# Kernel tuning notes

Hardware: AMD Instinct MI355X
Metric: run time of the kernel (lower is better)

## Reference

```python
import jax, jax.numpy as jnp
import numpy as np

N_NODES = 50000
NEG_SLOPE_ATT = 0.2   # PyG GATConv default LeakyReLU slope for attention logits
NEG_SLOPE_ACT = 0.01  # nn.LeakyReLU default between layers


def _add_self_loops(src, dst, n):
    loop = jnp.arange(n, dtype=src.dtype)
    return jnp.concatenate([src, loop]), jnp.concatenate([dst, loop])


def gat_conv(x, W, a_src, a_dst, b, src, dst, n):
    # x: [N, Cin], W: [Cin, Cout], a_src/a_dst: [Cout], b: [Cout]
    h = x @ W                                   # [N, Cout]
    alpha_src = h @ a_src                       # [N]
    alpha_dst = h @ a_dst                       # [N]
    e = jax.nn.leaky_relu(alpha_src[src] + alpha_dst[dst], NEG_SLOPE_ATT)  # [E]
    # segment softmax over incoming edges of each dst node
    m = jax.ops.segment_max(e, dst, num_segments=n)      # [N]
    ex = jnp.exp(e - m[dst])                              # [E]
    s = jax.ops.segment_sum(ex, dst, num_segments=n)      # [N] (>0: self-loops)
    alpha = ex / s[dst]                                   # [E]
    out = jax.ops.segment_sum(h[src] * alpha[:, None], dst, num_segments=n)
    return out + b


def setup_inputs() -> dict:
    key = jax.random.key(0)
    ks = jax.random.split(key, 20)
    n, e = N_NODES, 800000
    cin, h1, h2, cout = 64, 128, 64, 32
    d = {
        "x": jax.random.normal(ks[0], (n, cin), jnp.float32),
        "edge_index": jax.random.randint(ks[1], (2, e), 0, n, jnp.int64),
    }
    dims = [(cin, h1), (h1, h2), (h2, h1), (h1, cout)]
    for i, (ci, co) in enumerate(dims, 1):
        g = 1.0 / np.sqrt(ci)
        d[f"W{i}"] = jax.random.normal(ks[2 + 4 * i], (ci, co), jnp.float32) * g
        d[f"a{i}s"] = jax.random.normal(ks[3 + 4 * i], (co,), jnp.float32) * 0.1
        d[f"a{i}d"] = jax.random.normal(ks[4 + 4 * i], (co,), jnp.float32) * 0.1
        d[f"b{i}"] = jnp.zeros((co,), jnp.float32)
    return d


def reference(x, edge_index, W1, a1s, a1d, b1, W2, a2s, a2d, b2,
              W3, a3s, a3d, b3, W4, a4s, a4d, b4):
    n = x.shape[0]
    src, dst = _add_self_loops(edge_index[0], edge_index[1], n)
    act = lambda t: jax.nn.leaky_relu(t, NEG_SLOPE_ACT)
    h = act(gat_conv(x, W1, a1s, a1d, b1, src, dst, n))
    # dropout is identity at inference
    h = act(gat_conv(h, W2, a2s, a2d, b2, src, dst, n))
    h = act(gat_conv(h, W3, a3s, a3d, b3, src, dst, n))
    return gat_conv(h, W4, a4s, a4d, b4, src, dst, n)
```

## Files before the change

### kernel.cpp

```cpp
#include <hip/hip_runtime.h>
#include <hip/hip_fp16.h>

#define NEG_ATT 0.2f

typedef int v4i __attribute__((ext_vector_type(4)));


__global__ __launch_bounds__(256) void setup_k(int* cnt, int N, int NB,
                                               const float* __restrict__ W1, const float* __restrict__ a1s,
                                               const float* __restrict__ a1d, const float* __restrict__ W3,
                                               const float* __restrict__ a3s, const float* __restrict__ a3d,
                                               float* __restrict__ wa ) {
    int b = blockIdx.x;
    if (b < NB) {
        int i = b * 256 + threadIdx.x;
        if (i < N) cnt[i] = 0;
    } else {
        int t = threadIdx.x;
        int ci = t & 63;
        int which = t >> 6;
        const float* W = (which < 2) ? W1 : W3;
        const float* a = (which == 0) ? a1s : (which == 1) ? a1d : (which == 2) ? a3s : a3d;
        float s = 0.f;
        for (int co = 0; co < 128; ++co) s += W[ci * 128 + co] * a[co];
        wa[t] = s;
    }
}


__global__ __launch_bounds__(256) void scatter_gemv_k(const int* __restrict__ src, const int* __restrict__ dst,
                                                      int* cnt, int* __restrict__ col,
                                                      int E, int SB,
                                                      const float* __restrict__ X,
                                                      const float* __restrict__ was, const float* __restrict__ wad,
                                                      float* __restrict__ as_, float* __restrict__ ad_,
                                                      __half* __restrict__ x16, int N) {
    if (blockIdx.x < SB) {
        int i4 = blockIdx.x * 256 + threadIdx.x;
        int E4 = E >> 2;
        if (i4 < E4) {
            v4i d4 = *(const v4i*)&dst[i4 * 4];
            v4i s4 = *(const v4i*)&src[i4 * 4];
            #pragma unroll
            for (int u = 0; u < 4; ++u) {
                int slot = atomicAdd(&cnt[d4[u]], 1);
                col[(d4[u] << 6) + slot] = s4[u];
            }
        }
        if (blockIdx.x == 0 && threadIdx.x < (E & 3)) {
            int i = (E & ~3) + threadIdx.x;
            int dd = dst[i];
            int slot = atomicAdd(&cnt[dd], 1);
            col[(dd << 6) + slot] = src[i];
        }
    } else {
        int wid  = ((blockIdx.x - SB) * 256 + threadIdx.x) >> 6;
        int lane = threadIdx.x & 63;
        if (wid >= N) return;
        float xv = X[(size_t)wid * 64 + lane];
        x16[(size_t)wid * 64 + lane] = __float2half(xv);
        float s1 = xv * was[lane];
        float s2 = xv * wad[lane];
        #pragma unroll
        for (int off = 32; off; off >>= 1) {
            s1 += __shfl_xor(s1, off);
            s2 += __shfl_xor(s2, off);
        }
        if (lane == 0) { as_[wid] = s1; ad_[wid] = s2; }
    }
}


__global__ __launch_bounds__(256) void gemm_wide_k(const __half* __restrict__ X16, const float* __restrict__ W,
                                                   const float* __restrict__ bias, __half* __restrict__ H16, int N) {
    __shared__ float Xs[128][68];
    __shared__ float Ws[64][128];
    int tid  = threadIdx.x;
    int row0 = blockIdx.x * 128;

    for (int i = tid; i < 2048; i += 256)
        *(float4*)&((float*)Ws)[i * 4] = *(const float4*)&W[i * 4];
    for (int i = tid; i < 2048; i += 256) {
        int r = i >> 4, k4 = i & 15;
        int gr = row0 + r;
        float4 v = {0.f, 0.f, 0.f, 0.f};
        if (gr < N) {
            uint2 pk = *(const uint2*)&X16[(size_t)gr * 64 + k4 * 4];
            float2 f0 = __half22float2(*(__half2*)&pk.x);
            float2 f1 = __half22float2(*(__half2*)&pk.y);
            v = make_float4(f0.x, f0.y, f1.x, f1.y);
        }
        *(float4*)&Xs[r][k4 * 4] = v;
    }
    __syncthreads();

    int ct = tid & 15;
    int rt = tid >> 4;
    float acc[8][8] = {};
    for (int k = 0; k < 64; k += 4) {
        float4 w0a = *(float4*)&Ws[k][ct * 8],     w0b = *(float4*)&Ws[k][ct * 8 + 4];
        float4 w1a = *(float4*)&Ws[k + 1][ct * 8], w1b = *(float4*)&Ws[k + 1][ct * 8 + 4];
        float4 w2a = *(float4*)&Ws[k + 2][ct * 8], w2b = *(float4*)&Ws[k + 2][ct * 8 + 4];
        float4 w3a = *(float4*)&Ws[k + 3][ct * 8], w3b = *(float4*)&Ws[k + 3][ct * 8 + 4];
        #pragma unroll
        for (int i = 0; i < 8; ++i) {
            float4 xv = *(float4*)&Xs[rt + 16 * i][k];
            acc[i][0] += xv.x * w0a.x + xv.y * w1a.x + xv.z * w2a.x + xv.w * w3a.x;
            acc[i][1] += xv.x * w0a.y + xv.y * w1a.y + xv.z * w2a.y + xv.w * w3a.y;
            acc[i][2] += xv.x * w0a.z + xv.y * w1a.z + xv.z * w2a.z + xv.w * w3a.z;
            acc[i][3] += xv.x * w0a.w + xv.y * w1a.w + xv.z * w2a.w + xv.w * w3a.w;
            acc[i][4] += xv.x * w0b.x + xv.y * w1b.x + xv.z * w2b.x + xv.w * w3b.x;
            acc[i][5] += xv.x * w0b.y + xv.y * w1b.y + xv.z * w2b.y + xv.w * w3b.y;
            acc[i][6] += xv.x * w0b.z + xv.y * w1b.z + xv.z * w2b.z + xv.w * w3b.z;
            acc[i][7] += xv.x * w0b.w + xv.y * w1b.w + xv.z * w2b.w + xv.w * w3b.w;
        }
    }

    float bv[8];
    #pragma unroll
    for (int j = 0; j < 8; ++j) bv[j] = bias[ct * 8 + j];

    #pragma unroll
    for (int i = 0; i < 8; ++i) {
        int gr = row0 + rt + 16 * i;
        if (gr < N) {
            float o[8];
            #pragma unroll
            for (int j = 0; j < 8; ++j) {
                float v = acc[i][j] + bv[j];
                o[j] = v > 0.f ? v : 0.01f * v;
            }
            __half2 h0 = __floats2half2_rn(o[0], o[1]);
            __half2 h1 = __floats2half2_rn(o[2], o[3]);
            __half2 h2 = __floats2half2_rn(o[4], o[5]);
            __half2 h3 = __floats2half2_rn(o[6], o[7]);
            uint4 pk = { *(unsigned*)&h0, *(unsigned*)&h1, *(unsigned*)&h2, *(unsigned*)&h3 };
            *(uint4*)&H16[(size_t)gr * 128 + ct * 8] = pk;
        }
    }
}


template <int CIN, int COUT>
__global__ __launch_bounds__(256) void gemm_k(const __half* __restrict__ X16, const float* __restrict__ W,
                                              const float* __restrict__ a_s, const float* __restrict__ a_d,
                                              __half* __restrict__ Hh, float* __restrict__ as_,
                                              float* __restrict__ ad_, int N) {
    constexpr int RB  = (CIN == 128 && COUT == 64) ? 32 : 64;
    constexpr int NCT = COUT / 4;
    constexpr int NRT = 256 / NCT;
    constexpr int RT  = RB / NRT;
    constexpr int XP  = CIN + 4;
    __shared__ float Xs[RB][XP];
    __shared__ float Ws[CIN][COUT];
    int tid  = threadIdx.x;
    int row0 = blockIdx.x * RB;

    for (int i = tid; i < CIN * COUT / 4; i += 256)
        *(float4*)&((float*)Ws)[i * 4] = *(const float4*)&W[i * 4];
    for (int i = tid; i < RB * CIN / 4; i += 256) {
        int r = i / (CIN / 4), k4 = i % (CIN / 4);
        int gr = row0 + r;
        float4 v = {0.f, 0.f, 0.f, 0.f};
        if (gr < N) {
            uint2 pk = *(const uint2*)&X16[(size_t)gr * CIN + k4 * 4];
            float2 f0 = __half22float2(*(__half2*)&pk.x);
            float2 f1 = __half22float2(*(__half2*)&pk.y);
            v = make_float4(f0.x, f0.y, f1.x, f1.y);
        }
        *(float4*)&Xs[r][k4 * 4] = v;
    }
    __syncthreads();

    int ct = tid % NCT;
    int rt = tid / NCT;
    float acc[RT][4] = {};
    for (int k = 0; k < CIN; k += 4) {
        float4 w0 = *(float4*)&Ws[k][ct * 4];
        float4 w1 = *(float4*)&Ws[k + 1][ct * 4];
        float4 w2 = *(float4*)&Ws[k + 2][ct * 4];
        float4 w3 = *(float4*)&Ws[k + 3][ct * 4];
        #pragma unroll
        for (int i = 0; i < RT; ++i) {
            float4 xv = *(float4*)&Xs[rt + i * NRT][k];
            acc[i][0] += xv.x * w0.x + xv.y * w1.x + xv.z * w2.x + xv.w * w3.x;
            acc[i][1] += xv.x * w0.y + xv.y * w1.y + xv.z * w2.y + xv.w * w3.y;
            acc[i][2] += xv.x * w0.z + xv.y * w1.z + xv.z * w2.z + xv.w * w3.z;
            acc[i][3] += xv.x * w0.w + xv.y * w1.w + xv.z * w2.w + xv.w * w3.w;
        }
    }

    float asv[4], adv[4];
    #pragma unroll
    for (int j = 0; j < 4; ++j) { asv[j] = a_s[ct * 4 + j]; adv[j] = a_d[ct * 4 + j]; }

    #pragma unroll
    for (int i = 0; i < RT; ++i) {
        int gr = row0 + rt + i * NRT;
        float s1 = acc[i][0] * asv[0] + acc[i][1] * asv[1] + acc[i][2] * asv[2] + acc[i][3] * asv[3];
        float s2 = acc[i][0] * adv[0] + acc[i][1] * adv[1] + acc[i][2] * adv[2] + acc[i][3] * adv[3];
        #pragma unroll
        for (int off = 1; off < NCT; off <<= 1) {
            s1 += __shfl_xor(s1, off);
            s2 += __shfl_xor(s2, off);
        }
        if (gr < N) {
            __half2 p0 = __floats2half2_rn(acc[i][0], acc[i][1]);
            __half2 p1 = __floats2half2_rn(acc[i][2], acc[i][3]);
            uint2 pk = { *(unsigned*)&p0, *(unsigned*)&p1 };
            *(uint2*)&Hh[(size_t)gr * COUT + ct * 4] = pk;
            if (ct == 0) { as_[gr] = s1; ad_[gr] = s2; }
        }
    }
}


template <int C, int MODE>
__global__ __launch_bounds__(256) void agg_k(const __half* __restrict__ Hg, const float* __restrict__ as_,
                                             const float* __restrict__ ad_, const int* __restrict__ deg,
                                             const int* __restrict__ col, const float* __restrict__ bias,
                                             const float* __restrict__ was, const float* __restrict__ wad,
                                             float* __restrict__ outf, __half* __restrict__ outh,
                                             float* __restrict__ oas, float* __restrict__ oad, int N) {
    __shared__ int2 sw[4][64];
    int wid  = (blockIdx.x * 256 + threadIdx.x) >> 6;
    int lane = threadIdx.x & 63;
    int wvi  = threadIdx.x >> 6;
    if (wid >= N) return;
    float adi = ad_[wid];
    int dg = deg[wid];
    float a0 = 0.f, a1 = 0.f, b0 = 0.f, b1 = 0.f;
    const int sub  = lane >> 5, c32 = lane & 31;
    const int quad = lane >> 4, c16 = lane & 15;

    int s_l = 0; float w_l = 0.f;
    if (lane < dg) {
        s_l = col[(wid << 6) + lane];
        float e = as_[s_l] + adi;
        e = e > 0.f ? e : NEG_ATT * e;
        w_l = __expf(e);
    }
    sw[wvi][lane] = make_int2(s_l, __float_as_int(w_l));

    float es = as_[wid] + adi;
    es = es > 0.f ? es : NEG_ATT * es;
    float ws = __expf(es);
    float denom = w_l + ((lane == 0) ? ws : 0.f);
    if (C == 64) {
        if (!sub) {
            float2 f = __half22float2(*(const __half2*)&Hg[((size_t)wid << 6) + 2 * c32]);
            a0 += ws * f.x; a1 += ws * f.y;
        }
    } else {
        if (!quad) {
            float2 f = __half22float2(*(const __half2*)&Hg[((size_t)wid << 5) + 2 * c16]);
            a0 += ws * f.x; a1 += ws * f.y;
        }
    }

    auto g64 = [&](int j, auto NEhalf) {
        constexpr int M = decltype(NEhalf)::value;
        float2 hv[M]; float wv[M];
        #pragma unroll
        for (int u = 0; u < M; ++u) {
            int2 p = sw[wvi][j + 2 * u + sub];
            wv[u] = __int_as_float(p.y);
            hv[u] = __half22float2(*(const __half2*)&Hg[((size_t)p.x << 6) + 2 * c32]);
        }
        #pragma unroll
        for (int u = 0; u < M; ++u) {
            if (u & 1) { b0 += wv[u] * hv[u].x; b1 += wv[u] * hv[u].y; }
            else       { a0 += wv[u] * hv[u].x; a1 += wv[u] * hv[u].y; }
        }
    };
    auto g32 = [&](int j, auto NEq) {
        constexpr int M = decltype(NEq)::value;
        float2 hv[M]; float wv[M];
        #pragma unroll
        for (int u = 0; u < M; ++u) {
            int2 p = sw[wvi][j + 4 * u + quad];
            wv[u] = __int_as_float(p.y);
            hv[u] = __half22float2(*(const __half2*)&Hg[((size_t)p.x << 5) + 2 * c16]);
        }
        #pragma unroll
        for (int u = 0; u < M; ++u) {
            if (u & 1) { b0 += wv[u] * hv[u].x; b1 += wv[u] * hv[u].y; }
            else       { a0 += wv[u] * hv[u].x; a1 += wv[u] * hv[u].y; }
        }
    };

    int j = 0;
    if (C == 64) {
        for (; j + 16 <= dg; j += 16) g64(j, std::integral_constant<int, 8>{});
        int rem = dg - j;
        if (rem > 8) g64(j, std::integral_constant<int, 8>{});
        else if (rem > 4) g64(j, std::integral_constant<int, 4>{});
        else if (rem > 0) g64(j, std::integral_constant<int, 2>{});
    } else {
        for (; j + 16 <= dg; j += 16) g32(j, std::integral_constant<int, 4>{});
        int rem = dg - j;
        if (rem > 8) g32(j, std::integral_constant<int, 4>{});
        else if (rem > 4) g32(j, std::integral_constant<int, 2>{});
        else if (rem > 0) g32(j, std::integral_constant<int, 1>{});
    }

    float f0 = a0 + b0, f1 = a1 + b1;
    if (C == 32) { f0 += __shfl_xor(f0, 16); f1 += __shfl_xor(f1, 16); }
    f0 += __shfl_xor(f0, 32); f1 += __shfl_xor(f1, 32);
    #pragma unroll
    for (int off = 32; off; off >>= 1) denom += __shfl_xor(denom, off);

    float inv = 1.f / denom;
    float v0 = f0 * inv, v1 = f1 * inv;

    if (MODE == 0) {
        if (!sub) {
            __half2 p = __floats2half2_rn(v0, v1);
            *(__half2*)&outh[((size_t)wid << 6) + 2 * c32] = p;
        }
    } else if (MODE == 1) {
        float2 bb = *(const float2*)&bias[2 * c32];
        v0 += bb.x; v1 += bb.y;
        v0 = v0 > 0.f ? v0 : 0.01f * v0;
        v1 = v1 > 0.f ? v1 : 0.01f * v1;
        if (!sub) {
            __half2 p = __floats2half2_rn(v0, v1);
            *(__half2*)&outh[((size_t)wid << 6) + 2 * c32] = p;
        }
        float2 wsv = *(const float2*)&was[2 * c32];
        float2 wdv = *(const float2*)&wad[2 * c32];
        float s1 = v0 * wsv.x + v1 * wsv.y;
        float s2 = v0 * wdv.x + v1 * wdv.y;
        #pragma unroll
        for (int off = 16; off; off >>= 1) {
            s1 += __shfl_xor(s1, off);
            s2 += __shfl_xor(s2, off);
        }
        if (lane == 0) { oas[wid] = s1; oad[wid] = s2; }
    } else {
        if (!quad) {
            float2 bb = *(const float2*)&bias[2 * c16];
            float2 o = {v0 + bb.x, v1 + bb.y};
            *(float2*)&outf[((size_t)wid << 5) + 2 * c16] = o;
        }
    }
}


extern "C" void kernel_launch(void* const* d_in, const int* in_sizes, int n_in,
                              void* d_out, int out_size, void* d_ws, size_t ws_size,
                              hipStream_t stream) {
    const float* x  = (const float*)d_in[0];
    const int* ei   = (const int*)d_in[1];
    const float* W1 = (const float*)d_in[2];
    const float* a1s = (const float*)d_in[3];
    const float* a1d = (const float*)d_in[4];
    const float* b1  = (const float*)d_in[5];
    const float* W2 = (const float*)d_in[6];
    const float* a2s = (const float*)d_in[7];
    const float* a2d = (const float*)d_in[8];
    const float* b2  = (const float*)d_in[9];
    const float* W3 = (const float*)d_in[10];
    const float* a3s = (const float*)d_in[11];
    const float* a3d = (const float*)d_in[12];
    const float* b3  = (const float*)d_in[13];
    const float* W4 = (const float*)d_in[14];
    const float* a4s = (const float*)d_in[15];
    const float* a4d = (const float*)d_in[16];
    const float* b4  = (const float*)d_in[17];

    const int N = in_sizes[0] / 64;
    const int E = in_sizes[1] / 2;
    const int* src = ei;
    const int* dst = ei + E;

    float* asA  = (float*)d_ws;
    float* adA  = asA + N;
    float* asB  = adA + N;
    float* adB  = asB + N;
    float* wa   = adB + N;
    int* cnt    = (int*)(wa + 256);
    int* col    = cnt + N;
    __half* x16 = (__half*)(col + (size_t)N * 64);
    __half* g1  = x16 + (size_t)N * 64;
    __half* g2  = g1 + (size_t)N * 64;
    __half* g3  = g2 + (size_t)N * 64;
    __half* g4  = g3 + (size_t)N * 64;

    const int NB = (N + 255) / 256;
    const int SB = ((E >> 2) + 255) / 256;
    const int NWAVE = (N * 64 + 255) / 256;

    setup_k<<<NB + 1, 256, 0, stream>>>(cnt, N, NB, W1, a1s, a1d, W3, a3s, a3d, wa);
    float* wa1s = wa, *wa1d = wa + 64, *wa3s = wa + 128, *wa3d = wa + 192;

    scatter_gemv_k<<<SB + NWAVE, 256, 0, stream>>>(src, dst, cnt, col, E, SB,
                                                   x, wa1s, wa1d, asA, adA, x16, N);

    agg_k<64, 0><<<NWAVE, 256, 0, stream>>>(x16, asA, adA, cnt, col, nullptr, nullptr, nullptr,
                                            nullptr, g3, nullptr, nullptr, N);
    gemm_wide_k<<<(N + 127) / 128, 256, 0, stream>>>(g3, W1, b1, g4, N);

    gemm_k<128, 64><<<(N + 31) / 32, 256, 0, stream>>>(g4, W2, a2s, a2d, g1, asB, adB, N);
    agg_k<64, 1><<<NWAVE, 256, 0, stream>>>(g1, asB, adB, cnt, col, b2, wa3s, wa3d,
                                            nullptr, g2, asA, adA, N);

    agg_k<64, 0><<<NWAVE, 256, 0, stream>>>(g2, asA, adA, cnt, col, nullptr, nullptr, nullptr,
                                            nullptr, g3, nullptr, nullptr, N);
    gemm_wide_k<<<(N + 127) / 128, 256, 0, stream>>>(g3, W3, b3, g4, N);

    gemm_k<128, 32><<<(N + 63) / 64, 256, 0, stream>>>(g4, W4, a4s, a4d, g1, asB, adB, N);
    agg_k<32, 2><<<NWAVE, 256, 0, stream>>>(g1, asB, adB, cnt, col, b4, nullptr, nullptr,
                                            (float*)d_out, nullptr, nullptr, nullptr, N);
}
```

Measured before the change: 252.7 us.

## Partition edge scatter by destination range, store 16-bit column indices, unroll gather

The CSR-building scatter now runs in 8 partitions, one per range of destination nodes. Each partition scans all edges and only handles those whose destination falls in its range, which keeps atomics and col writes localized, presumably per XCD. Column indices are stored as unsigned short instead of int, halving col traffic in the scatter and in every aggregation, which relies on N fitting in 16 bits (50000 does). The aggregation loop over neighbors is replaced by a few fixed-size unrolled gathers chosen by degree bucket, trading extra redundant work for fewer branches.

```diff
diff --git a/kernel.cpp b/kernel.cpp
--- a/kernel.cpp
+++ b/kernel.cpp
@@ -2,8 +2,6 @@
 #include <hip/hip_fp16.h>
 
 #define NEG_ATT 0.2f
-
-typedef int v4i __attribute__((ext_vector_type(4)));
 
 
 __global__ __launch_bounds__(256) void setup_k(int* cnt, int N, int NB,
@@ -29,29 +27,33 @@
 
 
 __global__ __launch_bounds__(256) void scatter_gemv_k(const int* __restrict__ src, const int* __restrict__ dst,
-                                                      int* cnt, int* __restrict__ col,
-                                                      int E, int SB,
+                                                      int* cnt, unsigned short* __restrict__ col,
+                                                      int E, int step, int SB, int iters4,
                                                       const float* __restrict__ X,
                                                       const float* __restrict__ was, const float* __restrict__ wad,
                                                       float* __restrict__ as_, float* __restrict__ ad_,
                                                       __half* __restrict__ x16, int N) {
     if (blockIdx.x < SB) {
-        int i4 = blockIdx.x * 256 + threadIdx.x;
+        int part = blockIdx.x & 7;
+        int lo = part * step, hi = lo + step;
+        int tg = (blockIdx.x >> 3) * 256 + threadIdx.x;
+        int stride = (SB >> 3) * 256;
+        const int4* dst4 = (const int4*)dst;
         int E4 = E >> 2;
-        if (i4 < E4) {
-            v4i d4 = *(const v4i*)&dst[i4 * 4];
-            v4i s4 = *(const v4i*)&src[i4 * 4];
-            #pragma unroll
-            for (int u = 0; u < 4; ++u) {
-                int slot = atomicAdd(&cnt[d4[u]], 1);
-                col[(d4[u] << 6) + slot] = s4[u];
+        for (int it = 0; it < iters4; ++it) {
+            int i4 = tg + it * stride;
+            if (i4 < E4) {
+                int4 d4 = dst4[i4];
+                int base = i4 << 2;
+                if (d4.x >= lo && d4.x < hi) { int s = atomicAdd(&cnt[d4.x], 1); col[(d4.x << 6) + s] = (unsigned short)src[base]; }
+                if (d4.y >= lo && d4.y < hi) { int s = atomicAdd(&cnt[d4.y], 1); col[(d4.y << 6) + s] = (unsigned short)src[base + 1]; }
+                if (d4.z >= lo && d4.z < hi) { int s = atomicAdd(&cnt[d4.z], 1); col[(d4.z << 6) + s] = (unsigned short)src[base + 2]; }
+                if (d4.w >= lo && d4.w < hi) { int s = atomicAdd(&cnt[d4.w], 1); col[(d4.w << 6) + s] = (unsigned short)src[base + 3]; }
             }
         }
-        if (blockIdx.x == 0 && threadIdx.x < (E & 3)) {
-            int i = (E & ~3) + threadIdx.x;
+        for (int i = (E & ~3) + tg; i < E; i += stride) {
             int dd = dst[i];
-            int slot = atomicAdd(&cnt[dd], 1);
-            col[(dd << 6) + slot] = src[i];
+            if (dd >= lo && dd < hi) { int s = atomicAdd(&cnt[dd], 1); col[(dd << 6) + s] = (unsigned short)src[i]; }
         }
     } else {
         int wid  = ((blockIdx.x - SB) * 256 + threadIdx.x) >> 6;
@@ -218,7 +220,7 @@
 template <int C, int MODE>
 __global__ __launch_bounds__(256) void agg_k(const __half* __restrict__ Hg, const float* __restrict__ as_,
                                              const float* __restrict__ ad_, const int* __restrict__ deg,
-                                             const int* __restrict__ col, const float* __restrict__ bias,
+                                             const unsigned short* __restrict__ col, const float* __restrict__ bias,
                                              const float* __restrict__ was, const float* __restrict__ wad,
                                              float* __restrict__ outf, __half* __restrict__ outh,
                                              float* __restrict__ oas, float* __restrict__ oad, int N) {
@@ -289,19 +291,15 @@
         }
     };
 
-    int j = 0;
     if (C == 64) {
-        for (; j + 16 <= dg; j += 16) g64(j, std::integral_constant<int, 8>{});
-        int rem = dg - j;
-        if (rem > 8) g64(j, std::integral_constant<int, 8>{});
-        else if (rem > 4) g64(j, std::integral_constant<int, 4>{});
-        else if (rem > 0) g64(j, std::integral_constant<int, 2>{});
+        if (dg <= 8)       g64(0, std::integral_constant<int, 4>{});
+        else if (dg <= 16) g64(0, std::integral_constant<int, 8>{});
+        else if (dg <= 32) g64(0, std::integral_constant<int, 16>{});
+        else { g64(0, std::integral_constant<int, 16>{}); g64(32, std::integral_constant<int, 16>{}); }
     } else {
-        for (; j + 16 <= dg; j += 16) g32(j, std::integral_constant<int, 4>{});
-        int rem = dg - j;
-        if (rem > 8) g32(j, std::integral_constant<int, 4>{});
-        else if (rem > 4) g32(j, std::integral_constant<int, 2>{});
-        else if (rem > 0) g32(j, std::integral_constant<int, 1>{});
+        if (dg <= 16)      g32(0, std::integral_constant<int, 4>{});
+        else if (dg <= 32) g32(0, std::integral_constant<int, 8>{});
+        else { g32(0, std::integral_constant<int, 8>{}); g32(32, std::integral_constant<int, 8>{}); }
     }
 
     float f0 = a0 + b0, f1 = a1 + b1;
@@ -380,7 +378,7 @@
     float* adB  = asB + N;
     float* wa   = adB + N;
     int* cnt    = (int*)(wa + 256);
-    int* col    = cnt + N;
+    unsigned short* col = (unsigned short*)(cnt + N);
     __half* x16 = (__half*)(col + (size_t)N * 64);
     __half* g1  = x16 + (size_t)N * 64;
     __half* g2  = g1 + (size_t)N * 64;
@@ -388,13 +386,15 @@
     __half* g4  = g3 + (size_t)N * 64;
 
     const int NB = (N + 255) / 256;
-    const int SB = ((E >> 2) + 255) / 256;
+    const int STEP = (N + 7) / 8;
+    const int SB = 2048;
+    const int ITERS4 = ((E >> 2) + (SB / 8) * 256 - 1) / ((SB / 8) * 256);
     const int NWAVE = (N * 64 + 255) / 256;
 
     setup_k<<<NB + 1, 256, 0, stream>>>(cnt, N, NB, W1, a1s, a1d, W3, a3s, a3d, wa);
     float* wa1s = wa, *wa1d = wa + 64, *wa3s = wa + 128, *wa3d = wa + 192;
 
-    scatter_gemv_k<<<SB + NWAVE, 256, 0, stream>>>(src, dst, cnt, col, E, SB,
+    scatter_gemv_k<<<SB + NWAVE, 256, 0, stream>>>(src, dst, cnt, col, E, STEP, SB, ITERS4,
                                                    x, wa1s, wa1d, asA, adA, x16, N);
 
     agg_k<64, 0><<<NWAVE, 256, 0, stream>>>(x16, asA, adA, cnt, col, nullptr, nullptr, nullptr,
```

Result: faster. 243.5 us, median of 2 (-3.6%).
